# Kernel tuning notes

Measured on AMD Instinct MI355X. Metric: run time of the kernel, lower is better.

The kernel has to match this reference:

```python
import jax, jax.numpy as jnp
import numpy as np

# DnlsLoss config (init kwargs)
WS, WT, PS, K, STRIDE0 = 9, 1, 7, 10, 4
NEPOCHS, K_DECAY = 100, 1.0
B, T, C, H, W = 1, 5, 3, 256, 256


def setup_inputs():
    key = jax.random.key(0)
    k0, k1, k2, k3 = jax.random.split(key, 4)
    noisy = jax.random.uniform(k0, (B, T, C, H, W), jnp.float32)
    deno = jax.random.uniform(k1, (B, T, C, H, W), jnp.float32)
    fflow = jax.random.normal(k2, (B, T, 2, H, W), jnp.float32) * 2.0
    bflow = jax.random.normal(k3, (B, T, 2, H, W), jnp.float32) * 2.0
    return {"noisy": noisy, "deno": deno, "fflow": fflow, "bflow": bflow, "curr_epoch": 0}


def _patch_gather(vid, t, h, w, ps):
    # vid: [B,T,H,W,C]; t/h/w: int32 [B, ...]; returns [B, ..., ps, ps, C]
    Bv, Tv, Hv, Wv, Cv = vid.shape
    po = jnp.arange(ps)
    hh = jnp.clip(h[..., None, None] + po[:, None], 0, Hv - 1)
    ww = jnp.clip(w[..., None, None] + po[None, :], 0, Wv - 1)
    tt = t[..., None, None]
    bb = jnp.arange(Bv).reshape((Bv,) + (1,) * (hh.ndim - 1))
    return vid[bb, tt, hh, ww]


def _forward(noisy, deno, fflow, bflow, k_eff):
    srch = noisy  # search_input == 'noisy'
    to_v = lambda v: jnp.transpose(v, (0, 1, 3, 4, 2))  # BTCHW -> BTHWC
    srch_v, deno_v, noisy_v = to_v(srch), to_v(deno), to_v(noisy)
    wr = WS // 2
    # query grid on stride0 lattice
    nH, nW = (H - 1) // STRIDE0 + 1, (W - 1) // STRIDE0 + 1
    tq, hq, wq = jnp.meshgrid(jnp.arange(T), jnp.arange(nH) * STRIDE0,
                              jnp.arange(nW) * STRIDE0, indexing='ij')
    tq, hq, wq = tq.reshape(-1), hq.reshape(-1), wq.reshape(-1)  # [Q]
    Q = tq.shape[0]
    bq = lambda x: jnp.broadcast_to(x[None], (B, Q))
    # one-step optical-flow window centers (wt = 1); flow channels = (dx, dy)
    fl_v = jnp.transpose(fflow, (0, 1, 3, 4, 2))  # [B,T,H,W,2]
    bl_v = jnp.transpose(bflow, (0, 1, 3, 4, 2))
    bb = jnp.arange(B)[:, None]
    ff = jax.lax.stop_gradient(jnp.round(fl_v[bb, tq[None], hq[None], wq[None]])).astype(jnp.int32)
    bf = jax.lax.stop_gradient(jnp.round(bl_v[bb, tq[None], hq[None], wq[None]])).astype(jnp.int32)
    # frame order [0, -1, +1]: self anchor lives in block 0
    t_cen = jnp.stack([bq(tq), bq(jnp.clip(tq - 1, 0, T - 1)), bq(jnp.clip(tq + 1, 0, T - 1))], -1)
    h_cen = jnp.stack([bq(hq), jnp.clip(bq(hq) + bf[..., 1], 0, H - 1), jnp.clip(bq(hq) + ff[..., 1], 0, H - 1)], -1)
    w_cen = jnp.stack([bq(wq), jnp.clip(bq(wq) + bf[..., 0], 0, W - 1), jnp.clip(bq(wq) + ff[..., 0], 0, W - 1)], -1)
    St = 2 * WT + 1
    # query patches of the search video
    qpatch = _patch_gather(srch_v, bq(tq), bq(hq), bq(wq), PS)  # [B,Q,ps,ps,C]
    offs = jnp.asarray(np.stack(np.meshgrid(np.arange(St), np.arange(WS) - wr,
                                            np.arange(WS) - wr, indexing='ij'), -1).reshape(-1, 3))

    def step(carry, off):
        dti, dh, dw = off[0], off[1], off[2]
        tc = jnp.take(t_cen, dti, axis=2)
        hc = jnp.clip(jnp.take(h_cen, dti, axis=2) + dh, 0, H - 1)
        wc = jnp.clip(jnp.take(w_cen, dti, axis=2) + dw, 0, W - 1)
        cp = _patch_gather(srch_v, tc, hc, wc, PS)
        d = jnp.sum((qpatch - cp) ** 2, axis=(-3, -2, -1))  # [B,Q]
        return carry, (d, tc, hc, wc)

    _, (D, Tc, Hc, Wc) = jax.lax.scan(step, 0, offs)  # each [N,B,Q]
    tr = lambda x: jnp.moveaxis(x, 0, -1)  # -> [B,Q,N]
    D, Tc, Hc, Wc = tr(D), tr(Tc), tr(Hc), tr(Wc)
    # anchored top-k smallest l2 (anchor_self=True): force self (dt=0, dh=dw=0) to slot 0
    self_idx = wr * WS + wr
    keys = D.at[..., self_idx].set(-jnp.inf)
    negv, idx = jax.lax.top_k(-keys, k_eff)
    dists = (-negv).at[..., 0].set(D[..., self_idx])  # [B,Q,K] (unused for 'l2' crit)
    ga = lambda x: jnp.take_along_axis(x, idx, axis=-1)
    tK, hK, wK = ga(Tc), ga(Hc), ga(Wc)  # neighbor inds [B,Q,K]
    # RefineSearch(wr=1, kr=1): re-evaluate l2 between deno queries and noisy keys at inds
    qp = _patch_gather(deno_v, bq(tq), bq(hq), bq(wq), PS)  # [B,Q,ps,ps,C]
    kp = _patch_gather(noisy_v, tK, hK, wK, PS)             # [B,Q,K,ps,ps,C]
    dists_r = jnp.sum((qp[:, :, None] - kp) ** 2, axis=(-3, -2, -1))  # [B,Q,K]
    # dist_crit == 'l2': mean over all but the anchored self column
    return jnp.mean(dists_r[..., 1:])


def reference(noisy, deno, fflow, bflow, curr_epoch):
    k_eff = max(int(K * ((NEPOCHS - curr_epoch) / NEPOCHS) * K_DECAY), 2)
    return _forward(noisy, deno, fflow, bflow, k_eff)
```

## Files before the change

### kernel.cpp

```cpp
#include <hip/hip_runtime.h>

#define WS 9
#define PS 7
#define KMAX 10
#define STRIDE0 4
#define NEPOCHS 100
#define BB 1
#define TT 5
#define CC 3
#define HH 256
#define WW 256
#define QQ (TT * 64 * 64)
#define NOFF 243
#define SELF_IDX 40
#define HW (HH * WW)
#define TSTR 20

typedef float f4a __attribute__((ext_vector_type(4)));
typedef float f4u __attribute__((ext_vector_type(4), aligned(4)));

static __device__ __forceinline__ int k_eff_from_epoch(int ep) {
    int k = (int)((double)KMAX * ((double)(NEPOCHS - ep) / (double)NEPOCHS));
    return k < 2 ? 2 : k;
}

template <int CTRL>
static __device__ __forceinline__ float dpp_add(float v) {
    const int x = __float_as_int(v);
    const int y = __builtin_amdgcn_update_dpp(0, x, CTRL, 0xF, 0xF, true);
    return v + __int_as_float(y);
}
static __device__ __forceinline__ float swz4_add(float v) {
    const int x = __float_as_int(v);
    const int y = __builtin_amdgcn_ds_swizzle(x, 0x101F);
    return v + __int_as_float(y);
}

__global__ __launch_bounds__(256) void dnls_query_kernel(
    const float* __restrict__ noisy, const float* __restrict__ deno,
    const float* __restrict__ fflow, const float* __restrict__ bflow,
    const int* __restrict__ ep_ptr, float* __restrict__ partial)
{
    const int tid  = threadIdx.x;
    const int wid  = tid >> 6;
    const int lane = tid & 63;
    const int sub  = lane & 7;
    const int q    = blockIdx.x * 4 + wid;
    const int tqi  = q >> 12;
    const int r0   = q & 4095;
    const int hq   = (r0 >> 6) * STRIDE0;
    const int wq   = (r0 & 63) * STRIDE0;
    const int k_eff = k_eff_from_epoch(ep_ptr[0]);

    __shared__ __align__(16) float tile[4][3][CC][15][TSTR];
    __shared__ float dpat[4][CC][PS][8];
    __shared__ float dists[4][256];

    const size_t bfo = (size_t)(tqi * 2) * HW + (size_t)hq * WW + wq;
    const int ifdx = (int)rintf(fflow[bfo]);
    const int ifdy = (int)rintf(fflow[bfo + HW]);
    const int ibdx = (int)rintf(bflow[bfo]);
    const int ibdy = (int)rintf(bflow[bfo + HW]);
    const int tc0 = tqi, tc1 = max(tqi - 1, 0), tc2 = min(tqi + 1, TT - 1);
    const int hv0 = hq, hv1 = min(max(hq + ibdy, 0), HH - 1), hv2 = min(max(hq + ifdy, 0), HH - 1);
    const int wv0 = wq, wv1 = min(max(wq + ibdx, 0), WW - 1), wv2 = min(max(wq + ifdx, 0), WW - 1);

    #pragma unroll
    for (int rr = 0; rr < 9; ++rr) {
        const int u = lane + rr * 64;
        if (u < 540) {
            const int p   = u / 60;
            const int rem = u - p * 60;
            const int row = rem >> 2, qd = rem & 3;
            const int dti = (p >= 6) ? 2 : (p >= 3 ? 1 : 0);
            const int c   = p - dti * 3;
            const int tcv = dti == 0 ? tc0 : (dti == 1 ? tc1 : tc2);
            const int hcv = dti == 0 ? hv0 : (dti == 1 ? hv1 : hv2);
            const int wcv = dti == 0 ? wv0 : (dti == 1 ? wv1 : wv2);
            const int h0  = max(hcv - 4, 0), w0 = max(wcv - 4, 0);
            const float* src = noisy + (size_t)(tcv * CC + c) * HW;
            f4a v;
            if (hcv <= HH - 11 && wcv <= WW - 12) {
                v = (f4a)(*(const f4u*)(src + (h0 + row) * WW + w0 + qd * 4));
            } else {
                const int rrow = min(h0 + row, HH - 1);
                const float* sr = src + rrow * WW;
                #pragma unroll
                for (int t = 0; t < 4; ++t)
                    v[t] = sr[min(w0 + min(qd * 4 + t, 14), WW - 1)];
            }
            *(f4a*)&tile[wid][dti][c][row][qd * 4] = v;
        }
    }
    #pragma unroll
    for (int rr = 0; rr < 3; ++rr) {
        const int u = lane + rr * 64;
        if (u < CC * PS * PS) {
            const int c = u / 49, ij = u - c * 49, i = ij / 7, j = ij - (ij / 7) * 7;
            dpat[wid][c][i][j] = deno[(size_t)(tqi * CC + c) * HW
                                 + min(hq + i, HH - 1) * WW + min(wq + j, WW - 1)];
        }
    }
    __builtin_amdgcn_wave_barrier();

    const int oh = min(hq, 4), ow = min(wq, 4);
    float qv[CC][8];
    #pragma unroll
    for (int c = 0; c < CC; ++c) {
        *(f4a*)&qv[c][0] = *(const f4a*)&tile[wid][0][c][oh + sub][ow];
        *(f4a*)&qv[c][4] = *(const f4a*)&tile[wid][0][c][oh + sub][ow + 4];
    }

    #pragma unroll
    for (int it = 0; it < 4; ++it) {
        const int g = it * 8 + (lane >> 3);
        if (g < 27) {
            const int dti = (g >= 18) ? 2 : (g >= 9 ? 1 : 0);
            const int dh  = g - 9 * dti;
            const int hcv = dti == 0 ? hv0 : (dti == 1 ? hv1 : hv2);
            const int wcv = dti == 0 ? wv0 : (dti == 1 ? wv1 : wv2);
            float acc[9];
            #pragma unroll
            for (int dw = 0; dw < 9; ++dw) acc[dw] = 0.f;
            if (sub < PS) {
                if (hcv >= 4 && wcv >= 4) {
                    const int r = dh + sub;
                    #pragma unroll
                    for (int c = 0; c < CC; ++c) {
                        float tv[16];
                        *(f4a*)&tv[0]  = *(const f4a*)&tile[wid][dti][c][r][0];
                        *(f4a*)&tv[4]  = *(const f4a*)&tile[wid][dti][c][r][4];
                        *(f4a*)&tv[8]  = *(const f4a*)&tile[wid][dti][c][r][8];
                        *(f4a*)&tv[12] = *(const f4a*)&tile[wid][dti][c][r][12];
                        #pragma unroll
                        for (int dw = 0; dw < 9; ++dw) {
                            #pragma unroll
                            for (int j = 0; j < 7; ++j) {
                                const float d = qv[c][j] - tv[dw + j];
                                acc[dw] = fmaf(d, d, acc[dw]);
                            }
                        }
                    }
                } else {
                    const int h0 = max(hcv - 4, 0), w0 = max(wcv - 4, 0);
                    const int hc = min(max(hcv + dh - 4, 0), HH - 1);
                    const int r  = min(hc + sub, HH - 1) - h0;
                    #pragma unroll
                    for (int c = 0; c < CC; ++c) {
                        #pragma unroll
                        for (int dw = 0; dw < 9; ++dw) {
                            const int wc = min(max(wcv + dw - 4, 0), WW - 1);
                            #pragma unroll
                            for (int j = 0; j < 7; ++j) {
                                const int col = min(wc + j, WW - 1) - w0;
                                const float d = qv[c][j] - tile[wid][dti][c][r][col];
                                acc[dw] = fmaf(d, d, acc[dw]);
                            }
                        }
                    }
                }
            }
            #pragma unroll
            for (int dw = 0; dw < 9; ++dw) {
                float v = acc[dw];
                v = dpp_add<0xB1>(v);
                v = dpp_add<0x4E>(v);
                v = swz4_add(v);
                acc[dw] = v;
            }
            if (sub == 0) {
                #pragma unroll
                for (int dw = 0; dw < 9; ++dw) dists[wid][g * 9 + dw] = acc[dw];
            }
        }
    }
    __builtin_amdgcn_wave_barrier();

    const float* dq = dists[wid];
    float dv[4]; int dn[4];
    #pragma unroll
    for (int kk = 0; kk < 4; ++kk) {
        const int n = lane + kk * 64;
        float v = (n < NOFF) ? dq[n] : INFINITY;
        if (n == SELF_IDX) v = -INFINITY;
        dv[kk] = v; dn[kk] = n;
    }
    int seln[KMAX];
    #pragma unroll
    for (int k = 0; k < KMAX; ++k) {
        float bv = dv[0]; int bi = dn[0];
        #pragma unroll
        for (int kk = 1; kk < 4; ++kk)
            if (dv[kk] < bv || (dv[kk] == bv && dn[kk] < bi)) { bv = dv[kk]; bi = dn[kk]; }
        #pragma unroll
        for (int off = 32; off > 0; off >>= 1) {
            const float ov = __shfl_xor(bv, off);
            const int   oi = __shfl_xor(bi, off);
            if (ov < bv || (ov == bv && oi < bi)) { bv = ov; bi = oi; }
        }
        seln[k] = bi;
        #pragma unroll
        for (int kk = 0; kk < 4; ++kk) if (dn[kk] == bi) dv[kk] = INFINITY;
    }

    float part = 0.f;
    const int nref = (k_eff - 1) * 49;
    for (int u = lane; u < nref; u += 64) {
        const int kk = u / 49 + 1;
        const int ij = u - (kk - 1) * 49;
        const int i = ij / 7, j = ij - (ij / 7) * 7;
        int n = seln[1];
        #pragma unroll
        for (int t = 2; t < KMAX; ++t) if (kk == t) n = seln[t];
        const int dti = (n >= 162) ? 2 : (n >= 81 ? 1 : 0);
        const int rr  = n - dti * 81;
        const int dh  = rr / 9;
        const int dw  = rr - dh * 9;
        const int hcv = dti == 0 ? hv0 : (dti == 1 ? hv1 : hv2);
        const int wcv = dti == 0 ? wv0 : (dti == 1 ? wv1 : wv2);
        const int h0  = max(hcv - 4, 0), w0 = max(wcv - 4, 0);
        const int hc  = min(max(hcv + dh - 4, 0), HH - 1);
        const int wc  = min(max(wcv + dw - 4, 0), WW - 1);
        const int row = min(hc + i, HH - 1) - h0;
        const int col = min(wc + j, WW - 1) - w0;
        #pragma unroll
        for (int c = 0; c < CC; ++c) {
            const float d = dpat[wid][c][i][j] - tile[wid][dti][c][row][col];
            part = fmaf(d, d, part);
        }
    }

    #pragma unroll
    for (int off = 32; off > 0; off >>= 1) part += __shfl_xor(part, off);
    if (lane == 0) partial[q] = part;
}

__global__ __launch_bounds__(1024) void dnls_reduce_kernel(
    const float* __restrict__ partial, int n,
    const int* __restrict__ ep_ptr, float* __restrict__ out)
{
    const int tid = threadIdx.x;
    double acc = 0.0;
    for (int i = tid; i < n; i += 1024) acc += (double)partial[i];
    __shared__ double red[1024];
    red[tid] = acc;
    __syncthreads();
    for (int s = 512; s > 0; s >>= 1) {
        if (tid < s) red[tid] += red[tid + s];
        __syncthreads();
    }
    if (tid == 0) {
        const int k_eff = k_eff_from_epoch(ep_ptr[0]);
        out[0] = (float)(red[0] / ((double)n * (double)(k_eff - 1)));
    }
}

extern "C" void kernel_launch(void* const* d_in, const int* in_sizes, int n_in,
                              void* d_out, int out_size, void* d_ws, size_t ws_size,
                              hipStream_t stream) {
    const float* noisy = (const float*)d_in[0];
    const float* deno  = (const float*)d_in[1];
    const float* fflow = (const float*)d_in[2];
    const float* bflow = (const float*)d_in[3];
    const int*   ep    = (const int*)d_in[4];
    float* partial = (float*)d_ws;
    float* out = (float*)d_out;

    dnls_query_kernel<<<(BB * QQ) / 4, 256, 0, stream>>>(noisy, deno, fflow, bflow, ep, partial);
    dnls_reduce_kernel<<<1, 1024, 0, stream>>>(partial, BB * QQ, ep, out);
}
```

Baseline: 138.0 us.

## Swizzle LDS tile layout to remove padding and restructure refine loop

Shrinks the shared-memory tile row stride from 20 to 16 floats and applies an XOR swizzle on the 16-byte quad index by row, intended to keep LDS vector reads free of bank conflicts while cutting LDS footprint. The tile load loop is restructured so each pattern uses 60 lanes. The refinement stage now loops over neighbours with a wave-uniform index (readfirstlane), and the deno patch values are cached in registers per lane. This drops the per-element div/mod and select chains, but leaves 15 of 64 lanes idle in that stage.

Result: slower. 190.0 us (+37.7%).

```diff
diff --git a/kernel.cpp b/kernel.cpp
--- a/kernel.cpp
+++ b/kernel.cpp
@@ -14,7 +14,6 @@
 #define NOFF 243
 #define SELF_IDX 40
 #define HW (HH * WW)
-#define TSTR 20
 
 typedef float f4a __attribute__((ext_vector_type(4)));
 typedef float f4u __attribute__((ext_vector_type(4), aligned(4)));
@@ -52,9 +51,9 @@
     const int wq   = (r0 & 63) * STRIDE0;
     const int k_eff = k_eff_from_epoch(ep_ptr[0]);
 
-    __shared__ __align__(16) float tile[4][3][CC][15][TSTR];
-    __shared__ float dpat[4][CC][PS][8];
-    __shared__ float dists[4][256];
+    __shared__ __align__(16) float tile[4][9][15][16];
+    __shared__ float dpat[4][147];
+    __shared__ float dists[4][243];
 
     const size_t bfo = (size_t)(tqi * 2) * HW + (size_t)hq * WW + wq;
     const int ifdx = (int)rintf(fflow[bfo]);
@@ -66,18 +65,15 @@
     const int wv0 = wq, wv1 = min(max(wq + ibdx, 0), WW - 1), wv2 = min(max(wq + ifdx, 0), WW - 1);
 
     #pragma unroll
-    for (int rr = 0; rr < 9; ++rr) {
-        const int u = lane + rr * 64;
-        if (u < 540) {
-            const int p   = u / 60;
-            const int rem = u - p * 60;
-            const int row = rem >> 2, qd = rem & 3;
-            const int dti = (p >= 6) ? 2 : (p >= 3 ? 1 : 0);
-            const int c   = p - dti * 3;
-            const int tcv = dti == 0 ? tc0 : (dti == 1 ? tc1 : tc2);
-            const int hcv = dti == 0 ? hv0 : (dti == 1 ? hv1 : hv2);
-            const int wcv = dti == 0 ? wv0 : (dti == 1 ? wv1 : wv2);
-            const int h0  = max(hcv - 4, 0), w0 = max(wcv - 4, 0);
+    for (int p = 0; p < 9; ++p) {
+        const int dti = p / 3, c = p - dti * 3;
+        const int tcv = dti == 0 ? tc0 : (dti == 1 ? tc1 : tc2);
+        const int hcv = dti == 0 ? hv0 : (dti == 1 ? hv1 : hv2);
+        const int wcv = dti == 0 ? wv0 : (dti == 1 ? wv1 : wv2);
+        const int h0  = max(hcv - 4, 0), w0 = max(wcv - 4, 0);
+        if (lane < 60) {
+            const int row = lane >> 2, qd = lane & 3;
+            const int sq  = qd ^ (row & 3);
             const float* src = noisy + (size_t)(tcv * CC + c) * HW;
             f4a v;
             if (hcv <= HH - 11 && wcv <= WW - 12) {
@@ -89,26 +85,31 @@
                 for (int t = 0; t < 4; ++t)
                     v[t] = sr[min(w0 + min(qd * 4 + t, 14), WW - 1)];
             }
-            *(f4a*)&tile[wid][dti][c][row][qd * 4] = v;
+            *(f4a*)&tile[wid][p][row][sq * 4] = v;
         }
     }
     #pragma unroll
     for (int rr = 0; rr < 3; ++rr) {
         const int u = lane + rr * 64;
-        if (u < CC * PS * PS) {
+        if (u < 147) {
             const int c = u / 49, ij = u - c * 49, i = ij / 7, j = ij - (ij / 7) * 7;
-            dpat[wid][c][i][j] = deno[(size_t)(tqi * CC + c) * HW
-                                 + min(hq + i, HH - 1) * WW + min(wq + j, WW - 1)];
+            dpat[wid][u] = deno[(size_t)(tqi * CC + c) * HW
+                           + min(hq + i, HH - 1) * WW + min(wq + j, WW - 1)];
         }
     }
     __builtin_amdgcn_wave_barrier();
 
     const int oh = min(hq, 4), ow = min(wq, 4);
     float qv[CC][8];
-    #pragma unroll
-    for (int c = 0; c < CC; ++c) {
-        *(f4a*)&qv[c][0] = *(const f4a*)&tile[wid][0][c][oh + sub][ow];
-        *(f4a*)&qv[c][4] = *(const f4a*)&tile[wid][0][c][oh + sub][ow + 4];
+    {
+        const int r  = oh + sub;
+        const int sw = r & 3;
+        const int q0 = ow >> 2;
+        #pragma unroll
+        for (int c = 0; c < CC; ++c) {
+            *(f4a*)&qv[c][0] = *(const f4a*)&tile[wid][c][r][(q0 ^ sw) * 4];
+            *(f4a*)&qv[c][4] = *(const f4a*)&tile[wid][c][r][((q0 + 1) ^ sw) * 4];
+        }
     }
 
     #pragma unroll
@@ -124,14 +125,16 @@
             for (int dw = 0; dw < 9; ++dw) acc[dw] = 0.f;
             if (sub < PS) {
                 if (hcv >= 4 && wcv >= 4) {
-                    const int r = dh + sub;
+                    const int r  = dh + sub;
+                    const int sw = r & 3;
                     #pragma unroll
                     for (int c = 0; c < CC; ++c) {
+                        const float* tp = &tile[wid][dti * 3 + c][r][0];
                         float tv[16];
-                        *(f4a*)&tv[0]  = *(const f4a*)&tile[wid][dti][c][r][0];
-                        *(f4a*)&tv[4]  = *(const f4a*)&tile[wid][dti][c][r][4];
-                        *(f4a*)&tv[8]  = *(const f4a*)&tile[wid][dti][c][r][8];
-                        *(f4a*)&tv[12] = *(const f4a*)&tile[wid][dti][c][r][12];
+                        *(f4a*)&tv[0]  = *(const f4a*)(tp + ((0 ^ sw) << 2));
+                        *(f4a*)&tv[4]  = *(const f4a*)(tp + ((1 ^ sw) << 2));
+                        *(f4a*)&tv[8]  = *(const f4a*)(tp + ((2 ^ sw) << 2));
+                        *(f4a*)&tv[12] = *(const f4a*)(tp + ((3 ^ sw) << 2));
                         #pragma unroll
                         for (int dw = 0; dw < 9; ++dw) {
                             #pragma unroll
@@ -145,15 +148,17 @@
                     const int h0 = max(hcv - 4, 0), w0 = max(wcv - 4, 0);
                     const int hc = min(max(hcv + dh - 4, 0), HH - 1);
                     const int r  = min(hc + sub, HH - 1) - h0;
+                    const int swb = (r & 3) << 2;
                     #pragma unroll
                     for (int c = 0; c < CC; ++c) {
+                        const float* tp = &tile[wid][dti * 3 + c][r][0];
                         #pragma unroll
                         for (int dw = 0; dw < 9; ++dw) {
                             const int wc = min(max(wcv + dw - 4, 0), WW - 1);
                             #pragma unroll
                             for (int j = 0; j < 7; ++j) {
                                 const int col = min(wc + j, WW - 1) - w0;
-                                const float d = qv[c][j] - tile[wid][dti][c][r][col];
+                                const float d = qv[c][j] - tp[col ^ swb];
                                 acc[dw] = fmaf(d, d, acc[dw]);
                             }
                         }
@@ -203,30 +208,34 @@
         for (int kk = 0; kk < 4; ++kk) if (dn[kk] == bi) dv[kk] = INFINITY;
     }
 
+    const int li = lane / 7, lj = lane - (lane / 7) * 7;
+    float dpr[CC];
+    #pragma unroll
+    for (int c = 0; c < CC; ++c) dpr[c] = (lane < 49) ? dpat[wid][c * 49 + lane] : 0.f;
     float part = 0.f;
-    const int nref = (k_eff - 1) * 49;
-    for (int u = lane; u < nref; u += 64) {
-        const int kk = u / 49 + 1;
-        const int ij = u - (kk - 1) * 49;
-        const int i = ij / 7, j = ij - (ij / 7) * 7;
-        int n = seln[1];
-        #pragma unroll
-        for (int t = 2; t < KMAX; ++t) if (kk == t) n = seln[t];
-        const int dti = (n >= 162) ? 2 : (n >= 81 ? 1 : 0);
-        const int rr  = n - dti * 81;
-        const int dh  = rr / 9;
-        const int dw  = rr - dh * 9;
-        const int hcv = dti == 0 ? hv0 : (dti == 1 ? hv1 : hv2);
-        const int wcv = dti == 0 ? wv0 : (dti == 1 ? wv1 : wv2);
-        const int h0  = max(hcv - 4, 0), w0 = max(wcv - 4, 0);
-        const int hc  = min(max(hcv + dh - 4, 0), HH - 1);
-        const int wc  = min(max(wcv + dw - 4, 0), WW - 1);
-        const int row = min(hc + i, HH - 1) - h0;
-        const int col = min(wc + j, WW - 1) - w0;
-        #pragma unroll
-        for (int c = 0; c < CC; ++c) {
-            const float d = dpat[wid][c][i][j] - tile[wid][dti][c][row][col];
-            part = fmaf(d, d, part);
+    #pragma unroll
+    for (int k = 1; k < KMAX; ++k) {
+        if (k < k_eff) {
+            const int n = __builtin_amdgcn_readfirstlane(seln[k]);
+            const int dti = (n >= 162) ? 2 : (n >= 81 ? 1 : 0);
+            const int rr  = n - dti * 81;
+            const int dh  = rr / 9;
+            const int dw  = rr - dh * 9;
+            const int hcv = dti == 0 ? hv0 : (dti == 1 ? hv1 : hv2);
+            const int wcv = dti == 0 ? wv0 : (dti == 1 ? wv1 : wv2);
+            const int h0  = max(hcv - 4, 0), w0 = max(wcv - 4, 0);
+            const int hc  = min(max(hcv + dh - 4, 0), HH - 1);
+            const int wc  = min(max(wcv + dw - 4, 0), WW - 1);
+            if (lane < 49) {
+                const int row = min(hc + li, HH - 1) - h0;
+                const int col = min(wc + lj, WW - 1) - w0;
+                const int sc  = col ^ ((row & 3) << 2);
+                #pragma unroll
+                for (int c = 0; c < CC; ++c) {
+                    const float d = dpr[c] - tile[wid][dti * 3 + c][row][sc];
+                    part = fmaf(d, d, part);
+                }
+            }
         }
     }
 
```

## Keep deno patch in registers, pack L2 FMAs, restructure refine loop per neighbor

Applied to the files above, without the earlier changes.

Each lane now loads its own deno pixel (one per lane for the 49 patch positions) into registers instead of staging the patch in shared memory. The dense distance loop is reordered so each query value is reused across packed two-wide FMAs, aiming for v_pk_fma on CDNA. The refine stage becomes a per-neighbor unrolled loop with the neighbor index made wave-uniform through readfirstlane, which removes the divides and select chains of the flattened loop. This trades some lane idleness (15 of 64 lanes idle in refine) and extra registers for less LDS traffic and fewer ALU ops.

Result: faster. 132.6 us (-3.8%).

```diff
diff --git a/kernel.cpp b/kernel.cpp
--- a/kernel.cpp
+++ b/kernel.cpp
@@ -18,6 +18,7 @@
 
 typedef float f4a __attribute__((ext_vector_type(4)));
 typedef float f4u __attribute__((ext_vector_type(4), aligned(4)));
+typedef float f2  __attribute__((ext_vector_type(2)));
 
 static __device__ __forceinline__ int k_eff_from_epoch(int ep) {
     int k = (int)((double)KMAX * ((double)(NEPOCHS - ep) / (double)NEPOCHS));
@@ -53,8 +54,7 @@
     const int k_eff = k_eff_from_epoch(ep_ptr[0]);
 
     __shared__ __align__(16) float tile[4][3][CC][15][TSTR];
-    __shared__ float dpat[4][CC][PS][8];
-    __shared__ float dists[4][256];
+    __shared__ float dists[4][243];
 
     const size_t bfo = (size_t)(tqi * 2) * HW + (size_t)hq * WW + wq;
     const int ifdx = (int)rintf(fflow[bfo]);
@@ -64,6 +64,15 @@
     const int tc0 = tqi, tc1 = max(tqi - 1, 0), tc2 = min(tqi + 1, TT - 1);
     const int hv0 = hq, hv1 = min(max(hq + ibdy, 0), HH - 1), hv2 = min(max(hq + ifdy, 0), HH - 1);
     const int wv0 = wq, wv1 = min(max(wq + ibdx, 0), WW - 1), wv2 = min(max(wq + ifdx, 0), WW - 1);
+
+    const int li = lane / 7, lj = lane - (lane / 7) * 7;
+    float dpr[CC];
+    {
+        const float* db = deno + (size_t)(tqi * CC) * HW
+                          + (size_t)min(hq + li, HH - 1) * WW + min(wq + lj, WW - 1);
+        #pragma unroll
+        for (int c = 0; c < CC; ++c) dpr[c] = (lane < 49) ? db[c * HW] : 0.f;
+    }
 
     #pragma unroll
     for (int rr = 0; rr < 9; ++rr) {
@@ -92,15 +101,6 @@
             *(f4a*)&tile[wid][dti][c][row][qd * 4] = v;
         }
     }
-    #pragma unroll
-    for (int rr = 0; rr < 3; ++rr) {
-        const int u = lane + rr * 64;
-        if (u < CC * PS * PS) {
-            const int c = u / 49, ij = u - c * 49, i = ij / 7, j = ij - (ij / 7) * 7;
-            dpat[wid][c][i][j] = deno[(size_t)(tqi * CC + c) * HW
-                                 + min(hq + i, HH - 1) * WW + min(wq + j, WW - 1)];
-        }
-    }
     __builtin_amdgcn_wave_barrier();
 
     const int oh = min(hq, 4), ow = min(wq, 4);
@@ -125,6 +125,8 @@
             if (sub < PS) {
                 if (hcv >= 4 && wcv >= 4) {
                     const int r = dh + sub;
+                    f2 a2[4] = { f2{0.f,0.f}, f2{0.f,0.f}, f2{0.f,0.f}, f2{0.f,0.f} };
+                    float a8 = 0.f;
                     #pragma unroll
                     for (int c = 0; c < CC; ++c) {
                         float tv[16];
@@ -133,14 +135,21 @@
                         *(f4a*)&tv[8]  = *(const f4a*)&tile[wid][dti][c][r][8];
                         *(f4a*)&tv[12] = *(const f4a*)&tile[wid][dti][c][r][12];
                         #pragma unroll
-                        for (int dw = 0; dw < 9; ++dw) {
+                        for (int j = 0; j < 7; ++j) {
+                            const float qj = qv[c][j];
                             #pragma unroll
-                            for (int j = 0; j < 7; ++j) {
-                                const float d = qv[c][j] - tv[dw + j];
-                                acc[dw] = fmaf(d, d, acc[dw]);
+                            for (int p = 0; p < 4; ++p) {
+                                f2 t; t[0] = tv[2 * p + j]; t[1] = tv[2 * p + 1 + j];
+                                const f2 d = qj - t;
+                                a2[p] = __builtin_elementwise_fma(d, d, a2[p]);
                             }
+                            const float ds = qj - tv[8 + j];
+                            a8 = fmaf(ds, ds, a8);
                         }
                     }
+                    #pragma unroll
+                    for (int p = 0; p < 4; ++p) { acc[2 * p] = a2[p][0]; acc[2 * p + 1] = a2[p][1]; }
+                    acc[8] = a8;
                 } else {
                     const int h0 = max(hcv - 4, 0), w0 = max(wcv - 4, 0);
                     const int hc = min(max(hcv + dh - 4, 0), HH - 1);
@@ -204,29 +213,28 @@
     }
 
     float part = 0.f;
-    const int nref = (k_eff - 1) * 49;
-    for (int u = lane; u < nref; u += 64) {
-        const int kk = u / 49 + 1;
-        const int ij = u - (kk - 1) * 49;
-        const int i = ij / 7, j = ij - (ij / 7) * 7;
-        int n = seln[1];
-        #pragma unroll
-        for (int t = 2; t < KMAX; ++t) if (kk == t) n = seln[t];
-        const int dti = (n >= 162) ? 2 : (n >= 81 ? 1 : 0);
-        const int rr  = n - dti * 81;
-        const int dh  = rr / 9;
-        const int dw  = rr - dh * 9;
-        const int hcv = dti == 0 ? hv0 : (dti == 1 ? hv1 : hv2);
-        const int wcv = dti == 0 ? wv0 : (dti == 1 ? wv1 : wv2);
-        const int h0  = max(hcv - 4, 0), w0 = max(wcv - 4, 0);
-        const int hc  = min(max(hcv + dh - 4, 0), HH - 1);
-        const int wc  = min(max(wcv + dw - 4, 0), WW - 1);
-        const int row = min(hc + i, HH - 1) - h0;
-        const int col = min(wc + j, WW - 1) - w0;
-        #pragma unroll
-        for (int c = 0; c < CC; ++c) {
-            const float d = dpat[wid][c][i][j] - tile[wid][dti][c][row][col];
-            part = fmaf(d, d, part);
+    #pragma unroll
+    for (int k = 1; k < KMAX; ++k) {
+        if (k < k_eff) {
+            const int n = __builtin_amdgcn_readfirstlane(seln[k]);
+            const int dti = (n >= 162) ? 2 : (n >= 81 ? 1 : 0);
+            const int rr  = n - dti * 81;
+            const int dh  = rr / 9;
+            const int dw  = rr - dh * 9;
+            const int hcv = dti == 0 ? hv0 : (dti == 1 ? hv1 : hv2);
+            const int wcv = dti == 0 ? wv0 : (dti == 1 ? wv1 : wv2);
+            const int h0  = max(hcv - 4, 0), w0 = max(wcv - 4, 0);
+            const int hc  = min(max(hcv + dh - 4, 0), HH - 1);
+            const int wc  = min(max(wcv + dw - 4, 0), WW - 1);
+            if (lane < 49) {
+                const int row = min(hc + li, HH - 1) - h0;
+                const int col = min(wc + lj, WW - 1) - w0;
+                #pragma unroll
+                for (int c = 0; c < CC; ++c) {
+                    const float d = dpr[c] - tile[wid][dti][c][row][col];
+                    part = fmaf(d, d, part);
+                }
+            }
         }
     }
 
```
